# Performance work log

Hardware: AMD Instinct MI355X
Metric: run time of the kernel (lower is better)

The kernel has to match this reference:

```python
import jax, jax.numpy as jnp
import numpy as np

D = 768; NH = 12; HD = D // NH; L = 12; NC = 27; PATCH = 16; MLP = 3072; PROJ = 512
IMG = 224; GRID = IMG // PATCH; HW = GRID * GRID; S = NC + HW
NEG = -1e9

def _ln(x, w, b):
    m = jnp.mean(x, -1, keepdims=True)
    v = jnp.mean(jnp.square(x - m), -1, keepdims=True)
    return (x - m) * jax.lax.rsqrt(v + 1e-5) * w + b

def _quick_gelu(x):
    return x * jax.nn.sigmoid(1.702 * x)

def _build_mask(attn_obj_masks, dtype):
    # CRIS block mask: cls<->cls blocked except self; cls->patch allowed only for
    # patches of that class; patch->cls blocked; patch->patch fully allowed.
    B = attn_obj_masks.shape[0]
    oh = jax.nn.one_hot(attn_obj_masks, NC, dtype=dtype)              # [B, HW, NC]
    T11 = jnp.broadcast_to(1.0 - jnp.eye(NC, dtype=dtype), (B, NC, NC))
    M13 = 1.0 - jnp.swapaxes(oh, 1, 2)                                # [B, NC, HW]
    top = jnp.concatenate([T11, M13], axis=2)
    bot = jnp.concatenate([jnp.ones((B, HW, NC), dtype), jnp.zeros((B, HW, HW), dtype)], axis=2)
    Mb = jnp.concatenate([top, bot], axis=1)                          # [B, S, S]
    return jnp.where(Mb == 1.0, jnp.asarray(NEG, dtype), jnp.asarray(0.0, dtype))

def reference(img, sents, attn_obj_masks, obj_masks, cls_tokens, patch_w, patch_b, pos_embed,
              ln1_w, ln1_b, qkv_w, qkv_b, out_w, out_b, ln2_w, ln2_b,
              mlp_w1, mlp_b1, mlp_w2, mlp_b2, ln_post_w, ln_post_b, proj):
    B = img.shape[0]
    sents = sents / jnp.linalg.norm(sents, axis=-1, keepdims=True)    # encode_text output, L2 normed
    mask = _build_mask(attn_obj_masks, img.dtype)                     # [B, S, S]
    # patch embedding (conv stride 16) -> [B, HW, D]
    p = jax.lax.conv_general_dilated(img, patch_w, (PATCH, PATCH), 'VALID',
                                     dimension_numbers=('NCHW', 'OIHW', 'NCHW'))
    p = p.reshape(B, D, HW).transpose(0, 2, 1) + patch_b
    x = jnp.concatenate([jnp.broadcast_to(cls_tokens, (B, NC, D)), p], axis=1) + pos_embed
    scale = 1.0 / np.sqrt(HD).astype(np.float32)
    def block(x, prm):
        l1w, l1b, qw, qb, ow, ob, l2w, l2b, w1, b1, w2, b2 = prm
        h = _ln(x, l1w, l1b)
        qkv = h @ qw + qb
        q, k, v = jnp.split(qkv, 3, axis=-1)
        q = q.reshape(B, S, NH, HD).transpose(0, 2, 1, 3)
        k = k.reshape(B, S, NH, HD).transpose(0, 2, 1, 3)
        v = v.reshape(B, S, NH, HD).transpose(0, 2, 1, 3)
        scores = jnp.einsum('bhqd,bhkd->bhqk', q, k) * scale + mask[:, None]
        a = jax.nn.softmax(scores, axis=-1)
        o = jnp.einsum('bhqk,bhkd->bhqd', a, v).transpose(0, 2, 1, 3).reshape(B, S, D)
        x = x + o @ ow + ob
        h = _ln(x, l2w, l2b)
        x = x + _quick_gelu(h @ w1 + b1) @ w2 + b2
        return x, None
    x, _ = jax.lax.scan(block, x, (ln1_w, ln1_b, qkv_w, qkv_b, out_w, out_b,
                                   ln2_w, ln2_b, mlp_w1, mlp_b1, mlp_w2, mlp_b2))
    tokens = _ln(x, ln_post_w, ln_post_b) @ proj                      # [B, S, PROJ]
    obj = tokens[:, :NC]
    obj = obj / jnp.linalg.norm(obj, axis=-1, keepdims=True)
    pred_id = jnp.einsum('bnd,bd->bn', obj, sents)                    # [B, NC]
    # per-class scatter loop == gather of pred_id by per-pixel class id
    pred = jnp.take_along_axis(pred_id, obj_masks.reshape(B, -1), axis=1).reshape(obj_masks.shape)
    return pred                                                       # [B, 224, 224]

def setup_inputs():
    B = 16; std = 0.02
    ks = jax.random.split(jax.random.key(0), 16)
    f = jax.random.normal
    return {
        'img': f(ks[0], (B, 3, IMG, IMG), jnp.float32),
        'sents': f(ks[1], (B, PROJ), jnp.float32),
        'attn_obj_masks': jax.random.randint(ks[2], (B, HW), 0, NC, jnp.int32),
        'obj_masks': jax.random.randint(ks[3], (B, IMG, IMG), 0, NC, jnp.int32),
        'cls_tokens': f(ks[4], (1, NC, D)) * std,
        'patch_w': f(ks[5], (D, 3, PATCH, PATCH)) * std,
        'patch_b': jnp.zeros((D,)),
        'pos_embed': f(ks[6], (S, D)) * std,
        'ln1_w': jnp.ones((L, D)), 'ln1_b': jnp.zeros((L, D)),
        'qkv_w': f(ks[7], (L, D, 3 * D)) * std, 'qkv_b': jnp.zeros((L, 3 * D)),
        'out_w': f(ks[8], (L, D, D)) * std, 'out_b': jnp.zeros((L, D)),
        'ln2_w': jnp.ones((L, D)), 'ln2_b': jnp.zeros((L, D)),
        'mlp_w1': f(ks[9], (L, D, MLP)) * std, 'mlp_b1': jnp.zeros((L, MLP)),
        'mlp_w2': f(ks[10], (L, MLP, D)) * std, 'mlp_b2': jnp.zeros((L, D)),
        'ln_post_w': jnp.ones((D,)), 'ln_post_b': jnp.zeros((D,)),
        'proj': f(ks[11], (D, PROJ)) * std,
    }
```

## Files before the change

kernel.cpp:

```cpp
#include <hip/hip_runtime.h>

#define DEV __device__ __forceinline__

typedef short bf16x8 __attribute__((ext_vector_type(8)));
typedef float f32x4 __attribute__((ext_vector_type(4)));
typedef int vi4 __attribute__((ext_vector_type(4)));
typedef unsigned uint2v __attribute__((ext_vector_type(2)));
typedef unsigned short u16;
typedef short short4v __attribute__((ext_vector_type(4)));

#define NEGV -1000000000.0f

DEV u16 f2bf(float f) {
  union { float f; unsigned u; } v; v.f = f;
  unsigned r = v.u + 0x7FFFu + ((v.u >> 16) & 1u);
  return (u16)(r >> 16);
}

DEV bf16x8 ld_bf8(const u16* p) {
  vi4 v = *(const vi4*)p;
  return __builtin_bit_cast(bf16x8, v);
}

DEV void gload_lds16(const u16* g, vi4* l) {
  __builtin_amdgcn_global_load_lds((const __attribute__((address_space(1))) void*)g,
                                   (__attribute__((address_space(3))) void*)l, 16, 0, 0);
}

DEV unsigned lds_off(const void* p) {
  return (unsigned)(unsigned long long)(const __attribute__((address_space(3))) void*)p;
}

DEV uint2v ds_tr16(unsigned byteaddr) {
  uint2v r;
  asm volatile("ds_read_b64_tr_b16 %0, %1" : "=v"(r) : "v"(byteaddr));
  return r;
}

template<int BN, int MODE, bool GELU, int KS>
__global__ __launch_bounds__(256) void gemm_bt(
    const u16* __restrict__ A, const u16* __restrict__ Bt,
    const float* __restrict__ bias,
    float* __restrict__ Cf, u16* __restrict__ Cb,
    int M, int N, int K, const float* __restrict__ pos, long pstride)
{
  constexpr int FJ = BN / 32;
  constexpr int LTOT = 4 + FJ;
  __shared__ vi4 As[2][1024];
  __shared__ vi4 Bs[2][BN * 8];

  int gx = gridDim.x, gy = gridDim.y;
  int nwg = gx * gy * (int)gridDim.z;
  int orig = blockIdx.x + gx * (blockIdx.y + gy * blockIdx.z);
  int qq = nwg >> 3, rr = nwg & 7;
  int xcd = orig & 7, off = orig >> 3;
  int id = (xcd < rr) ? xcd * (qq + 1) + off : rr * (qq + 1) + (xcd - rr) * qq + off;
  int bx = id % gx, rest = id / gx, by = rest % gy, bz = rest / gy;

  int tid = threadIdx.x, lane = tid & 63, wid = tid >> 6;
  int wm = wid >> 1, wn = wid & 1;
  int m0 = by * 128, n0 = bx * BN;
  int kBeg = (K / KS) * bz;
  int nT = (K / KS) >> 6;
  f32x4 acc[4][FJ] = {};

  auto STAGE = [&](int buf, int kk) {
    #pragma unroll
    for (int r = 0; r < 4; ++r) {
      int flat = r * 256 + tid;
      int row = flat >> 3, c = flat & 7;
      int cs = c ^ (row & 7);
      gload_lds16(A + (long)(m0 + row) * K + kk + cs * 8, &As[buf][r * 256 + wid * 64]);
    }
    #pragma unroll
    for (int r = 0; r < FJ; ++r) {
      int flat = r * 256 + tid;
      int row = flat >> 3, c = flat & 7;
      int cs = c ^ (row & 7);
      gload_lds16(Bt + (long)(n0 + row) * K + kk + cs * 8, &Bs[buf][r * 256 + wid * 64]);
    }
  };

  STAGE(0, kBeg);
  int cur = 0;
  for (int t = 0; t < nT; ++t) {
    if (t + 1 < nT) {
      STAGE(cur ^ 1, kBeg + (t + 1) * 64);
      asm volatile("s_waitcnt vmcnt(%0)" :: "i"(LTOT) : "memory");
    } else {
      asm volatile("s_waitcnt vmcnt(0)" ::: "memory");
    }
    __builtin_amdgcn_s_barrier();
    int cg = lane >> 4, l15 = lane & 15;
    #pragma unroll
    for (int ks = 0; ks < 2; ++ks) {
      bf16x8 af[4], bfr[FJ];
      #pragma unroll
      for (int i = 0; i < 4; ++i) {
        int ra = wm * 64 + i * 16 + l15;
        af[i] = __builtin_bit_cast(bf16x8, As[cur][ra * 8 + ((ks * 4 + cg) ^ (ra & 7))]);
      }
      #pragma unroll
      for (int j = 0; j < FJ; ++j) {
        int rb = wn * (BN / 2) + j * 16 + l15;
        bfr[j] = __builtin_bit_cast(bf16x8, Bs[cur][rb * 8 + ((ks * 4 + cg) ^ (rb & 7))]);
      }
      #pragma unroll
      for (int i = 0; i < 4; ++i)
        #pragma unroll
        for (int j = 0; j < FJ; ++j)
          acc[i][j] = __builtin_amdgcn_mfma_f32_16x16x32_bf16(af[i], bfr[j], acc[i][j], 0, 0, 0);
    }
    __builtin_amdgcn_s_barrier();
    cur ^= 1;
  }

  int cg = lane >> 4, l15 = lane & 15;
  float* Cfz = (MODE == 2 && KS > 1) ? Cf + (long)bz * pstride : Cf;
  #pragma unroll
  for (int i = 0; i < 4; ++i) {
    #pragma unroll
    for (int j = 0; j < FJ; ++j) {
      int col = n0 + wn * (BN / 2) + j * 16 + l15;
      float bv = bias ? bias[col] : 0.f;
      #pragma unroll
      for (int r = 0; r < 4; ++r) {
        int row = m0 + wm * 64 + i * 16 + cg * 4 + r;
        if (row < M) {
          float v = acc[i][j][r];
          if (KS == 1 || bz == 0) v += bv;
          if (GELU) v = v / (1.f + __expf(-1.702f * v));
          if (MODE == 0) Cb[(long)row * N + col] = f2bf(v);
          else if (MODE == 2) Cfz[(long)row * N + col] = v;
          else {
            int hw = row % 196;
            int xr = (row / 196) * 223 + 27 + hw;
            Cf[(long)xr * 768 + col] = v + pos[(27 + hw) * 768 + col];
          }
        }
      }
    }
  }
}

__global__ __launch_bounds__(256) void attn_kernel(
    const u16* __restrict__ QKV, const int* __restrict__ aom, u16* __restrict__ O)
{
  __shared__ vi4 Kl[224 * 8];
  __shared__ vi4 Vl[224 * 8];
  __shared__ int ml[196];
  int tid = threadIdx.x, lane = tid & 63, wid = tid >> 6;
  int qg = blockIdx.x, h = blockIdx.y, b = blockIdx.z;
  long rowbase = (long)b * 223;
  #pragma unroll
  for (int it = 0; it < 7; ++it) {
    int flat = it * 256 + tid;
    int s = flat >> 3, c = flat & 7;
    int cs = c ^ (s & 7);
    gload_lds16(QKV + (rowbase + s) * 2304 + 768 + h * 64 + cs * 8, &Kl[it * 256 + wid * 64]);
  }
  #pragma unroll
  for (int it = 0; it < 7; ++it) {
    int u = it * 256 + tid;
    int slin = u >> 3, inner = u & 7;
    int sk = slin >> 2, sdp = slin & 3;
    int s = sk * 4 + (inner >> 1);
    int c = ((sdp ^ (sk & 3)) << 1) | (inner & 1);
    gload_lds16(QKV + (rowbase + s) * 2304 + 1536 + h * 64 + c * 8, &Vl[it * 256 + wid * 64]);
  }
  for (int i = tid; i < 196; i += 256) ml[i] = aom[b * 196 + i];
  __syncthreads();

  int l15 = lane & 15, cg = lane >> 4;
  unsigned vbase = lds_off(Vl);
  #pragma unroll
  for (int rep = 0; rep < 2; ++rep) {
    int fo = wid * 2 + rep;
    if (fo >= 7) break;
    int qf = qg * 7 + fo;
    int q0 = qf * 16;
    int arow = q0 + l15; if (arow > 222) arow = 222;
    const u16* qb = QKV + (rowbase + arow) * 2304 + h * 64;
    bf16x8 aq0 = ld_bf8(qb + cg * 8);
    bf16x8 aq1 = ld_bf8(qb + 32 + cg * 8);

    f32x4 sc[14];
    #pragma unroll
    for (int kf = 0; kf < 14; ++kf) {
      int key = kf * 16 + l15;
      f32x4 a = {0.f, 0.f, 0.f, 0.f};
      bf16x8 bk0 = __builtin_bit_cast(bf16x8, Kl[key * 8 + (cg ^ (key & 7))]);
      bf16x8 bk1 = __builtin_bit_cast(bf16x8, Kl[key * 8 + ((4 + cg) ^ (key & 7))]);
      a = __builtin_amdgcn_mfma_f32_16x16x32_bf16(bk0, aq0, a, 0, 0, 0);
      a = __builtin_amdgcn_mfma_f32_16x16x32_bf16(bk1, aq1, a, 0, 0, 0);
      sc[kf] = a;
    }
    int q = q0 + l15;
    float mx = -3.4e38f;
    #pragma unroll
    for (int kf = 0; kf < 14; ++kf) {
      #pragma unroll
      for (int r = 0; r < 4; ++r) {
        int key = kf * 16 + cg * 4 + r;
        float mval;
        if (key >= 223) mval = NEGV;
        else if (q >= 27) mval = (key < 27) ? NEGV : 0.f;
        else if (key < 27) mval = (key == q) ? 0.f : NEGV;
        else mval = (ml[key - 27] == q) ? 0.f : NEGV;
        float sv = sc[kf][r] * 0.125f + mval;
        sc[kf][r] = sv;
        mx = fmaxf(mx, sv);
      }
    }
    mx = fmaxf(mx, __shfl_xor(mx, 16));
    mx = fmaxf(mx, __shfl_xor(mx, 32));
    float sum = 0.f;
    #pragma unroll
    for (int kf = 0; kf < 14; ++kf) {
      #pragma unroll
      for (int r = 0; r < 4; ++r) {
        float e = __expf(sc[kf][r] - mx);
        sc[kf][r] = e; sum += e;
      }
    }
    sum += __shfl_xor(sum, 16);
    sum += __shfl_xor(sum, 32);
    float inv = 1.f / sum;
    unsigned plo[14], phi[14];
    #pragma unroll
    for (int kf = 0; kf < 14; ++kf) {
      plo[kf] = (unsigned)f2bf(sc[kf][0] * inv) | ((unsigned)f2bf(sc[kf][1] * inv) << 16);
      phi[kf] = (unsigned)f2bf(sc[kf][2] * inv) | ((unsigned)f2bf(sc[kf][3] * inv) << 16);
    }
    f32x4 oacc[4] = {};
    #pragma unroll
    for (int ks = 0; ks < 7; ++ks) {
      uint2v vr[4][2];
      int sk0 = ks * 8 + cg * 2, sk1 = sk0 + 1;
      #pragma unroll
      for (int nf = 0; nf < 4; ++nf) {
        vr[nf][0] = ds_tr16(vbase + (unsigned)(((sk0 * 4 + (nf ^ (sk0 & 3))) << 7) + l15 * 8));
        vr[nf][1] = ds_tr16(vbase + (unsigned)(((sk1 * 4 + (nf ^ (sk1 & 3))) << 7) + l15 * 8));
      }
      int src0 = ((cg & 1) << 5) + l15, src1 = src0 + 16;
      int lo0 = __shfl((int)plo[2 * ks], src0),     hi0 = __shfl((int)phi[2 * ks], src0);
      int lo1 = __shfl((int)plo[2 * ks + 1], src0), hi1 = __shfl((int)phi[2 * ks + 1], src0);
      int lo0b = __shfl((int)plo[2 * ks], src1),     hi0b = __shfl((int)phi[2 * ks], src1);
      int lo1b = __shfl((int)plo[2 * ks + 1], src1), hi1b = __shfl((int)phi[2 * ks + 1], src1);
      bool hg = (cg >> 1) & 1;
      vi4 paw = { hg ? lo1 : lo0, hg ? hi1 : hi0, hg ? lo1b : lo0b, hg ? hi1b : hi0b };
      bf16x8 pa = __builtin_bit_cast(bf16x8, paw);
      asm volatile("s_waitcnt lgkmcnt(0)" ::: "memory");
      __builtin_amdgcn_sched_barrier(0);
      #pragma unroll
      for (int nf = 0; nf < 4; ++nf) {
        vi4 bw = { (int)vr[nf][0][0], (int)vr[nf][0][1], (int)vr[nf][1][0], (int)vr[nf][1][1] };
        oacc[nf] = __builtin_amdgcn_mfma_f32_16x16x32_bf16(pa, __builtin_bit_cast(bf16x8, bw), oacc[nf], 0, 0, 0);
      }
    }
    #pragma unroll
    for (int nf = 0; nf < 4; ++nf) {
      int d = h * 64 + nf * 16 + l15;
      #pragma unroll
      for (int r = 0; r < 4; ++r) {
        int qo = q0 + cg * 4 + r;
        if (qo < 223) O[(rowbase + qo) * 768 + d] = f2bf(oacc[nf][r]);
      }
    }
  }
}

template<int NADD, bool MAP27, bool WRITEX>
__global__ __launch_bounds__(256) void ln_kernel(
    const float* __restrict__ X, const float* __restrict__ P, long ps,
    float* __restrict__ Xout, u16* __restrict__ Hb,
    const float* __restrict__ w, const float* __restrict__ bb, int nrows)
{
  int row = blockIdx.x * 4 + (threadIdx.x >> 6);
  if (row >= nrows) return;
  int xr = MAP27 ? (row / 27) * 223 + (row % 27) : row;
  int l = threadIdx.x & 63;
  const float4* xp = (const float4*)(X + (long)xr * 768);
  float4 a = xp[l], c = xp[l + 64], d = xp[l + 128];
  if (NADD == 2) {
    const float4* p0 = (const float4*)(P + (long)xr * 768);
    const float4* p1 = (const float4*)(P + ps + (long)xr * 768);
    float4 u0 = p0[l], u1 = p0[l + 64], u2 = p0[l + 128];
    float4 v0 = p1[l], v1 = p1[l + 64], v2 = p1[l + 128];
    a.x += u0.x + v0.x; a.y += u0.y + v0.y; a.z += u0.z + v0.z; a.w += u0.w + v0.w;
    c.x += u1.x + v1.x; c.y += u1.y + v1.y; c.z += u1.z + v1.z; c.w += u1.w + v1.w;
    d.x += u2.x + v2.x; d.y += u2.y + v2.y; d.z += u2.z + v2.z; d.w += u2.w + v2.w;
  }
  if (WRITEX) {
    float4* xo = (float4*)(Xout + (long)xr * 768);
    xo[l] = a; xo[l + 64] = c; xo[l + 128] = d;
  }
  float s = a.x + a.y + a.z + a.w + c.x + c.y + c.z + c.w + d.x + d.y + d.z + d.w;
  #pragma unroll
  for (int t = 1; t < 64; t <<= 1) s += __shfl_xor(s, t);
  float mean = s * (1.f / 768.f);
  a.x -= mean; a.y -= mean; a.z -= mean; a.w -= mean;
  c.x -= mean; c.y -= mean; c.z -= mean; c.w -= mean;
  d.x -= mean; d.y -= mean; d.z -= mean; d.w -= mean;
  float q = a.x*a.x + a.y*a.y + a.z*a.z + a.w*a.w
          + c.x*c.x + c.y*c.y + c.z*c.z + c.w*c.w
          + d.x*d.x + d.y*d.y + d.z*d.z + d.w*d.w;
  #pragma unroll
  for (int t = 1; t < 64; t <<= 1) q += __shfl_xor(q, t);
  float rs = rsqrtf(q * (1.f / 768.f) + 1e-5f);
  const float4* wp = (const float4*)w;
  const float4* bp = (const float4*)bb;
  u16* out = Hb + (long)row * 768;
  float4 w0 = wp[l], w1 = wp[l + 64], w2 = wp[l + 128];
  float4 b0 = bp[l], b1 = bp[l + 64], b2 = bp[l + 128];
  short4v o;
  o[0] = (short)f2bf(a.x * rs * w0.x + b0.x); o[1] = (short)f2bf(a.y * rs * w0.y + b0.y);
  o[2] = (short)f2bf(a.z * rs * w0.z + b0.z); o[3] = (short)f2bf(a.w * rs * w0.w + b0.w);
  *(short4v*)(out + l * 4) = o;
  o[0] = (short)f2bf(c.x * rs * w1.x + b1.x); o[1] = (short)f2bf(c.y * rs * w1.y + b1.y);
  o[2] = (short)f2bf(c.z * rs * w1.z + b1.z); o[3] = (short)f2bf(c.w * rs * w1.w + b1.w);
  *(short4v*)(out + 256 + l * 4) = o;
  o[0] = (short)f2bf(d.x * rs * w2.x + b2.x); o[1] = (short)f2bf(d.y * rs * w2.y + b2.y);
  o[2] = (short)f2bf(d.z * rs * w2.z + b2.z); o[3] = (short)f2bf(d.w * rs * w2.w + b2.w);
  *(short4v*)(out + 512 + l * 4) = o;
}

__global__ __launch_bounds__(256) void transpose_w(
    const float* __restrict__ W, u16* __restrict__ WT, int K, int N, long sW, long sT)
{
  __shared__ float t[64][65];
  int z = blockIdx.z;
  W += (long)z * sW; WT += (long)z * sT;
  int n0 = blockIdx.x * 64, k0 = blockIdx.y * 64;
  #pragma unroll
  for (int i = 0; i < 4; ++i) {
    int flat = i * 256 + threadIdx.x;
    int r = flat >> 4, c = (flat & 15) * 4;
    float4 v = *(const float4*)(W + (long)(k0 + r) * N + n0 + c);
    t[r][c] = v.x; t[r][c + 1] = v.y; t[r][c + 2] = v.z; t[r][c + 3] = v.w;
  }
  __syncthreads();
  #pragma unroll
  for (int i = 0; i < 8; ++i) {
    int flat = i * 256 + threadIdx.x;
    int rn = flat >> 5, ck = (flat & 31) * 2;
    unsigned val = (unsigned)f2bf(t[ck][rn]) | ((unsigned)f2bf(t[ck + 1][rn]) << 16);
    *(unsigned*)(WT + (long)(n0 + rn) * K + k0 + ck) = val;
  }
}

__global__ void convert_bf16(const float* __restrict__ src, u16* __restrict__ dst, int n) {
  int i = blockIdx.x * 256 + threadIdx.x;
  if (i < n) dst[i] = f2bf(src[i]);
}

__global__ __launch_bounds__(192) void patch_extract(const float* __restrict__ img, u16* __restrict__ Xp) {
  int row = blockIdx.x;
  int t = threadIdx.x;
  int pair = t >> 2, part = t & 3;
  int cch = pair >> 4, kh = pair & 15;
  int b = row / 196, hw = row % 196, gh = hw / 14, gw = hw % 14;
  float4 v = *(const float4*)(img + ((long)(b * 3 + cch) * 224 + gh * 16 + kh) * 224 + gw * 16 + part * 4);
  short4v o;
  o[0] = (short)f2bf(v.x); o[1] = (short)f2bf(v.y); o[2] = (short)f2bf(v.z); o[3] = (short)f2bf(v.w);
  *(short4v*)(Xp + (long)row * 768 + pair * 16 + part * 4) = o;
}

__global__ void cls_pos_fill(const float* __restrict__ cls, const float* __restrict__ pos, float* __restrict__ x) {
  int i = blockIdx.x * 256 + threadIdx.x;
  if (i >= 16 * 27 * 768) return;
  int d = i % 768, t = i / 768, b = t / 27, s = t % 27;
  x[((long)b * 223 + s) * 768 + d] = cls[s * 768 + d] + pos[s * 768 + d];
}

__global__ __launch_bounds__(256) void sents_norm(const float* __restrict__ s, float* __restrict__ sn) {
  __shared__ float sb[4];
  int b = blockIdx.x, t = threadIdx.x;
  float v0 = s[b * 512 + t], v1 = s[b * 512 + t + 256];
  float q = v0 * v0 + v1 * v1;
  #pragma unroll
  for (int d = 1; d < 64; d <<= 1) q += __shfl_xor(q, d);
  if ((t & 63) == 0) sb[t >> 6] = q;
  __syncthreads();
  float inv = rsqrtf(sb[0] + sb[1] + sb[2] + sb[3]);
  sn[b * 512 + t] = v0 * inv;
  sn[b * 512 + t + 256] = v1 * inv;
}

__global__ __launch_bounds__(256) void obj_dot(const float* __restrict__ obj, const float* __restrict__ sn, float* __restrict__ pid) {
  __shared__ float sb[8];
  int r = blockIdx.x, t = threadIdx.x, b = r / 27;
  float v0 = obj[(long)r * 512 + t], v1 = obj[(long)r * 512 + t + 256];
  float w0 = sn[b * 512 + t], w1 = sn[b * 512 + t + 256];
  float q = v0 * v0 + v1 * v1;
  float dt = v0 * w0 + v1 * w1;
  #pragma unroll
  for (int d = 1; d < 64; d <<= 1) { q += __shfl_xor(q, d); dt += __shfl_xor(dt, d); }
  if ((t & 63) == 0) { sb[t >> 6] = q; sb[4 + (t >> 6)] = dt; }
  __syncthreads();
  if (t == 0) pid[r] = (sb[4] + sb[5] + sb[6] + sb[7]) * rsqrtf(sb[0] + sb[1] + sb[2] + sb[3]);
}

__global__ void gather_pred(const int* __restrict__ om, const float* __restrict__ pid, float* __restrict__ out) {
  int i = blockIdx.x * 256 + threadIdx.x;
  if (i >= 16 * 224 * 224) return;
  int b = i / (224 * 224);
  out[i] = pid[b * 27 + om[i]];
}

extern "C" void kernel_launch(void* const* d_in, const int* in_sizes, int n_in,
                              void* d_out, int out_size, void* d_ws, size_t ws_size,
                              hipStream_t stream) {
  const float* img     = (const float*)d_in[0];
  const float* sents   = (const float*)d_in[1];
  const int*   aom     = (const int*)d_in[2];
  const int*   omask   = (const int*)d_in[3];
  const float* cls     = (const float*)d_in[4];
  const float* patch_w = (const float*)d_in[5];
  const float* patch_b = (const float*)d_in[6];
  const float* pos     = (const float*)d_in[7];
  const float* ln1w    = (const float*)d_in[8];
  const float* ln1b    = (const float*)d_in[9];
  const float* qkvw    = (const float*)d_in[10];
  const float* qkvb    = (const float*)d_in[11];
  const float* outw    = (const float*)d_in[12];
  const float* outb    = (const float*)d_in[13];
  const float* ln2w    = (const float*)d_in[14];
  const float* ln2b    = (const float*)d_in[15];
  const float* m1w     = (const float*)d_in[16];
  const float* m1b     = (const float*)d_in[17];
  const float* m2w     = (const float*)d_in[18];
  const float* m2b     = (const float*)d_in[19];
  const float* lnpw    = (const float*)d_in[20];
  const float* lnpb    = (const float*)d_in[21];
  const float* projw   = (const float*)d_in[22];

  char* p = (char*)d_ws;
  auto alloc = [&](size_t bytes) { char* r = p; p += (bytes + 255) & ~(size_t)255; return r; };
  const long PS = 3584l * 768;
  float* x   = (float*)alloc(3568ul * 768 * 4);
  u16* H     = (u16*)alloc(3584ul * 768 * 2);
  u16* QKV   = (u16*)alloc(3584ul * 2304 * 2);
  u16* Obuf  = (u16*)alloc(3584ul * 768 * 2);
  u16* G     = (u16*)alloc(3584ul * 3072 * 2);
  float* Y   = (float*)alloc((size_t)PS * 2 * 4);
  float* Mp  = (float*)alloc((size_t)PS * 2 * 4);
  u16* PWc   = (u16*)alloc(768ul * 768 * 2);
  u16* PrT   = (u16*)alloc(512ul * 768 * 2);
  float* obj = (float*)alloc(432ul * 512 * 4);
  float* sn  = (float*)alloc(16ul * 512 * 4);
  float* pid = (float*)alloc(432ul * 4);

  const size_t wlayer = (2304ul * 768 + 768ul * 768 + 3072ul * 768 + 768ul * 3072) * 2;
  size_t used = (size_t)(p - (char*)d_ws);
  int nw = (ws_size >= used + 12 * wlayer + 65536) ? 12 : 1;
  const long sQ = 2304l * 768, sO = 768l * 768, s1 = 768l * 3072, s2 = 3072l * 768;
  u16* WqT = (u16*)alloc((size_t)sQ * 2 * nw);
  u16* WoT = (u16*)alloc((size_t)sO * 2 * nw);
  u16* W1T = (u16*)alloc((size_t)s1 * 2 * nw);
  u16* W2T = (u16*)alloc((size_t)s2 * 2 * nw);

  convert_bf16<<<2304, 256, 0, stream>>>(patch_w, PWc, 768 * 768);
  transpose_w<<<dim3(8, 12, 1), 256, 0, stream>>>(projw, PrT, 768, 512, 0, 0);
  if (nw == 12) {
    transpose_w<<<dim3(36, 12, 12), 256, 0, stream>>>(qkvw, WqT, 768, 2304, sQ, sQ);
    transpose_w<<<dim3(12, 12, 12), 256, 0, stream>>>(outw, WoT, 768, 768, sO, sO);
    transpose_w<<<dim3(48, 12, 12), 256, 0, stream>>>(m1w, W1T, 768, 3072, s1, s1);
    transpose_w<<<dim3(12, 48, 12), 256, 0, stream>>>(m2w, W2T, 3072, 768, s2, s2);
  }
  patch_extract<<<3136, 192, 0, stream>>>(img, H);
  cls_pos_fill<<<1296, 256, 0, stream>>>(cls, pos, x);
  gemm_bt<64, 3, false, 1><<<dim3(12, 25), 256, 0, stream>>>(H, PWc, patch_b, x, nullptr, 3136, 768, 768, pos, 0);

  for (int l = 0; l < 12; ++l) {
    u16 *wq, *wo, *w1, *w2;
    if (nw == 12) { wq = WqT + (long)l * sQ; wo = WoT + (long)l * sO; w1 = W1T + (long)l * s1; w2 = W2T + (long)l * s2; }
    else {
      wq = WqT; wo = WoT; w1 = W1T; w2 = W2T;
      transpose_w<<<dim3(36, 12, 1), 256, 0, stream>>>(qkvw + (long)l * sQ, wq, 768, 2304, 0, 0);
      transpose_w<<<dim3(12, 12, 1), 256, 0, stream>>>(outw + (long)l * sO, wo, 768, 768, 0, 0);
      transpose_w<<<dim3(48, 12, 1), 256, 0, stream>>>(m1w + (long)l * s1, w1, 768, 3072, 0, 0);
      transpose_w<<<dim3(12, 48, 1), 256, 0, stream>>>(m2w + (long)l * s2, w2, 3072, 768, 0, 0);
    }
    if (l == 0)
      ln_kernel<0, false, false><<<892, 256, 0, stream>>>(x, nullptr, 0, nullptr, H, ln1w, ln1b, 3568);
    else
      ln_kernel<2, false, true><<<892, 256, 0, stream>>>(x, Mp, PS, x, H, ln1w + l * 768, ln1b + l * 768, 3568);
    gemm_bt<128, 0, false, 1><<<dim3(18, 28), 256, 0, stream>>>(H, wq, qkvb + l * 2304, nullptr, QKV, 3568, 2304, 768, nullptr, 0);
    attn_kernel<<<dim3(2, 12, 16), 256, 0, stream>>>(QKV, aom, Obuf);
    gemm_bt<64, 2, false, 2><<<dim3(12, 28, 2), 256, 0, stream>>>(Obuf, wo, outb + l * 768, Y, nullptr, 3568, 768, 768, nullptr, PS);
    ln_kernel<2, false, true><<<892, 256, 0, stream>>>(x, Y, PS, x, H, ln2w + l * 768, ln2b + l * 768, 3568);
    gemm_bt<128, 0, true, 1><<<dim3(24, 28), 256, 0, stream>>>(H, w1, m1b + l * 3072, nullptr, G, 3568, 3072, 768, nullptr, 0);
    gemm_bt<64, 2, false, 2><<<dim3(12, 28, 2), 256, 0, stream>>>(G, w2, m2b + l * 768, Mp, nullptr, 3568, 768, 3072, nullptr, PS);
  }

  ln_kernel<2, true, false><<<108, 256, 0, stream>>>(x, Mp, PS, nullptr, H, lnpw, lnpb, 432);
  gemm_bt<64, 2, false, 1><<<dim3(8, 4), 256, 0, stream>>>(H, PrT, nullptr, obj, nullptr, 432, 512, 768, nullptr, 0);
  sents_norm<<<16, 256, 0, stream>>>(sents, sn);
  obj_dot<<<432, 256, 0, stream>>>(obj, sn, pid);
  gather_pred<<<3136, 256, 0, stream>>>(omask, pid, (float*)d_out);
}
```

Baseline: 2.150 ms.

## Fuse residual add into out-proj and MLP2 GEMM epilogues, drop split-K

The out-projection and second MLP GEMMs now add their results directly into the fp32 residual stream in the epilogue, instead of writing two split-K partial buffers that the following layernorm summed and wrote back. The layernorm kernel becomes a pure normalize pass that reads only x. This removes the partial-buffer traffic and the residual write inside the layernorm. In exchange, split-K is dropped for these GEMMs, so the grid has half as many workgroups and the K=3072 GEMM has longer per-block loops.

After: 2.361 ms. +9.9%, slower.

```diff
diff --git a/kernel.cpp b/kernel.cpp
--- a/kernel.cpp
+++ b/kernel.cpp
@@ -42,7 +42,7 @@
     const u16* __restrict__ A, const u16* __restrict__ Bt,
     const float* __restrict__ bias,
     float* __restrict__ Cf, u16* __restrict__ Cb,
-    int M, int N, int K, const float* __restrict__ pos, long pstride)
+    int M, int N, int K, const float* __restrict__ pos)
 {
   constexpr int FJ = BN / 32;
   constexpr int LTOT = 4 + FJ;
@@ -116,7 +116,6 @@
   }
 
   int cg = lane >> 4, l15 = lane & 15;
-  float* Cfz = (MODE == 2 && KS > 1) ? Cf + (long)bz * pstride : Cf;
   #pragma unroll
   for (int i = 0; i < 4; ++i) {
     #pragma unroll
@@ -127,11 +126,11 @@
       for (int r = 0; r < 4; ++r) {
         int row = m0 + wm * 64 + i * 16 + cg * 4 + r;
         if (row < M) {
-          float v = acc[i][j][r];
-          if (KS == 1 || bz == 0) v += bv;
+          float v = acc[i][j][r] + bv;
           if (GELU) v = v / (1.f + __expf(-1.702f * v));
           if (MODE == 0) Cb[(long)row * N + col] = f2bf(v);
-          else if (MODE == 2) Cfz[(long)row * N + col] = v;
+          else if (MODE == 1) Cf[(long)row * N + col] += v;
+          else if (MODE == 2) Cf[(long)row * N + col] = v;
           else {
             int hw = row % 196;
             int xr = (row / 196) * 223 + 27 + hw;
@@ -270,10 +269,9 @@
   }
 }
 
-template<int NADD, bool MAP27, bool WRITEX>
+template<bool MAP27>
 __global__ __launch_bounds__(256) void ln_kernel(
-    const float* __restrict__ X, const float* __restrict__ P, long ps,
-    float* __restrict__ Xout, u16* __restrict__ Hb,
+    const float* __restrict__ X, u16* __restrict__ Hb,
     const float* __restrict__ w, const float* __restrict__ bb, int nrows)
 {
   int row = blockIdx.x * 4 + (threadIdx.x >> 6);
@@ -282,19 +280,6 @@
   int l = threadIdx.x & 63;
   const float4* xp = (const float4*)(X + (long)xr * 768);
   float4 a = xp[l], c = xp[l + 64], d = xp[l + 128];
-  if (NADD == 2) {
-    const float4* p0 = (const float4*)(P + (long)xr * 768);
-    const float4* p1 = (const float4*)(P + ps + (long)xr * 768);
-    float4 u0 = p0[l], u1 = p0[l + 64], u2 = p0[l + 128];
-    float4 v0 = p1[l], v1 = p1[l + 64], v2 = p1[l + 128];
-    a.x += u0.x + v0.x; a.y += u0.y + v0.y; a.z += u0.z + v0.z; a.w += u0.w + v0.w;
-    c.x += u1.x + v1.x; c.y += u1.y + v1.y; c.z += u1.z + v1.z; c.w += u1.w + v1.w;
-    d.x += u2.x + v2.x; d.y += u2.y + v2.y; d.z += u2.z + v2.z; d.w += u2.w + v2.w;
-  }
-  if (WRITEX) {
-    float4* xo = (float4*)(Xout + (long)xr * 768);
-    xo[l] = a; xo[l + 64] = c; xo[l + 128] = d;
-  }
   float s = a.x + a.y + a.z + a.w + c.x + c.y + c.z + c.w + d.x + d.y + d.z + d.w;
   #pragma unroll
   for (int t = 1; t < 64; t <<= 1) s += __shfl_xor(s, t);
@@ -437,14 +422,11 @@
 
   char* p = (char*)d_ws;
   auto alloc = [&](size_t bytes) { char* r = p; p += (bytes + 255) & ~(size_t)255; return r; };
-  const long PS = 3584l * 768;
   float* x   = (float*)alloc(3568ul * 768 * 4);
   u16* H     = (u16*)alloc(3584ul * 768 * 2);
   u16* QKV   = (u16*)alloc(3584ul * 2304 * 2);
   u16* Obuf  = (u16*)alloc(3584ul * 768 * 2);
   u16* G     = (u16*)alloc(3584ul * 3072 * 2);
-  float* Y   = (float*)alloc((size_t)PS * 2 * 4);
-  float* Mp  = (float*)alloc((size_t)PS * 2 * 4);
   u16* PWc   = (u16*)alloc(768ul * 768 * 2);
   u16* PrT   = (u16*)alloc(512ul * 768 * 2);
   float* obj = (float*)alloc(432ul * 512 * 4);
@@ -470,7 +452,7 @@
   }
   patch_extract<<<3136, 192, 0, stream>>>(img, H);
   cls_pos_fill<<<1296, 256, 0, stream>>>(cls, pos, x);
-  gemm_bt<64, 3, false, 1><<<dim3(12, 25), 256, 0, stream>>>(H, PWc, patch_b, x, nullptr, 3136, 768, 768, pos, 0);
+  gemm_bt<64, 3, false, 1><<<dim3(12, 25), 256, 0, stream>>>(H, PWc, patch_b, x, nullptr, 3136, 768, 768, pos);
 
   for (int l = 0; l < 12; ++l) {
     u16 *wq, *wo, *w1, *w2;
@@ -482,20 +464,17 @@
       transpose_w<<<dim3(48, 12, 1), 256, 0, stream>>>(m1w + (long)l * s1, w1, 768, 3072, 0, 0);
       transpose_w<<<dim3(12, 48, 1), 256, 0, stream>>>(m2w + (long)l * s2, w2, 3072, 768, 0, 0);
     }
-    if (l == 0)
-      ln_kernel<0, false, false><<<892, 256, 0, stream>>>(x, nullptr, 0, nullptr, H, ln1w, ln1b, 3568);
-    else
-      ln_kernel<2, false, true><<<892, 256, 0, stream>>>(x, Mp, PS, x, H, ln1w + l * 768, ln1b + l * 768, 3568);
-    gemm_bt<128, 0, false, 1><<<dim3(18, 28), 256, 0, stream>>>(H, wq, qkvb + l * 2304, nullptr, QKV, 3568, 2304, 768, nullptr, 0);
+    ln_kernel<false><<<892, 256, 0, stream>>>(x, H, ln1w + l * 768, ln1b + l * 768, 3568);
+    gemm_bt<128, 0, false, 1><<<dim3(18, 28), 256, 0, stream>>>(H, wq, qkvb + l * 2304, nullptr, QKV, 3568, 2304, 768, nullptr);
     attn_kernel<<<dim3(2, 12, 16), 256, 0, stream>>>(QKV, aom, Obuf);
-    gemm_bt<64, 2, false, 2><<<dim3(12, 28, 2), 256, 0, stream>>>(Obuf, wo, outb + l * 768, Y, nullptr, 3568, 768, 768, nullptr, PS);
-    ln_kernel<2, false, true><<<892, 256, 0, stream>>>(x, Y, PS, x, H, ln2w + l * 768, ln2b + l * 768, 3568);
-    gemm_bt<128, 0, true, 1><<<dim3(24, 28), 256, 0, stream>>>(H, w1, m1b + l * 3072, nullptr, G, 3568, 3072, 768, nullptr, 0);
-    gemm_bt<64, 2, false, 2><<<dim3(12, 28, 2), 256, 0, stream>>>(G, w2, m2b + l * 768, Mp, nullptr, 3568, 768, 3072, nullptr, PS);
-  }
-
-  ln_kernel<2, true, false><<<108, 256, 0, stream>>>(x, Mp, PS, nullptr, H, lnpw, lnpb, 432);
-  gemm_bt<64, 2, false, 1><<<dim3(8, 4), 256, 0, stream>>>(H, PrT, nullptr, obj, nullptr, 432, 512, 768, nullptr, 0);
+    gemm_bt<64, 1, false, 1><<<dim3(12, 28), 256, 0, stream>>>(Obuf, wo, outb + l * 768, x, nullptr, 3568, 768, 768, nullptr);
+    ln_kernel<false><<<892, 256, 0, stream>>>(x, H, ln2w + l * 768, ln2b + l * 768, 3568);
+    gemm_bt<128, 0, true, 1><<<dim3(24, 28), 256, 0, stream>>>(H, w1, m1b + l * 3072, nullptr, G, 3568, 3072, 768, nullptr);
+    gemm_bt<64, 1, false, 1><<<dim3(12, 28), 256, 0, stream>>>(G, w2, m2b + l * 768, x, nullptr, 3568, 768, 3072, nullptr);
+  }
+
+  ln_kernel<true><<<108, 256, 0, stream>>>(x, H, lnpw, lnpb, 432);
+  gemm_bt<64, 2, false, 1><<<dim3(8, 4), 256, 0, stream>>>(H, PrT, nullptr, obj, nullptr, 432, 512, 768, nullptr);
   sents_norm<<<16, 256, 0, stream>>>(sents, sn);
   obj_dot<<<432, 256, 0, stream>>>(obj, sn, pid);
   gather_pred<<<3136, 256, 0, stream>>>(omask, pid, (float*)d_out);
```
